# Kernel optimization log

Measured on AMD Instinct MI355X. Metric: run time of the kernel, lower is better.

## Reference

```python
import jax, jax.numpy as jnp
import numpy as np
from jax import lax

DIM = 96
B, S = 2, 48
EPS_LN = 1e-6
EPS_GRN = 1e-6


def setup_inputs() -> dict:
    key = jax.random.key(0)
    ks = jax.random.split(key, 11)
    d, h = DIM, 4 * DIM
    return {
        "x": jax.random.normal(ks[0], (B, d, S, S, S), jnp.float32),
        "dw_w": jax.random.normal(ks[1], (d, 1, 7, 7, 7), jnp.float32) * 0.05,  # (O, I/groups, kD,kH,kW)
        "dw_b": jax.random.normal(ks[2], (d,), jnp.float32) * 0.02,
        "ln_w": jnp.ones((d,), jnp.float32),
        "ln_b": jnp.zeros((d,), jnp.float32),
        "w1": jax.random.normal(ks[3], (d, h), jnp.float32) * 0.02,
        "b1": jax.random.normal(ks[4], (h,), jnp.float32) * 0.02,
        "grn_w": jax.random.normal(ks[5], (h,), jnp.float32) * 0.02,
        "grn_b": jax.random.normal(ks[6], (h,), jnp.float32) * 0.02,
        "w2": jax.random.normal(ks[7], (h, d), jnp.float32) * 0.02,
        "b2": jax.random.normal(ks[8], (d,), jnp.float32) * 0.02,
    }


def reference(x, dw_w, dw_b, ln_w, ln_b, w1, b1, grn_w, grn_b, w2, b2):
    # depthwise 7x7x7 conv, padding 3, groups = channels; x: (B, C, D, H, W)
    y = lax.conv_general_dilated(
        x, dw_w, window_strides=(1, 1, 1), padding=[(3, 3)] * 3,
        dimension_numbers=("NCDHW", "OIDHW", "NCDHW"), feature_group_count=DIM,
    ) + dw_b[None, :, None, None, None]
    # channels_last: (B, D, H, W, C)
    h = jnp.transpose(y, (0, 2, 3, 4, 1))
    # LayerNorm over channel dim
    mu = jnp.mean(h, axis=-1, keepdims=True)
    var = jnp.mean((h - mu) ** 2, axis=-1, keepdims=True)
    h = (h - mu) * lax.rsqrt(var + EPS_LN) * ln_w + ln_b
    # pointwise MLP expand + GELU (exact, erf-based, like torch)
    h = jnp.einsum("bdhwc,ce->bdhwe", h, w1) + b1
    h = jax.nn.gelu(h, approximate=False)
    # GRN: global L2 norm over spatial dims (1,2,3), per channel
    g = jnp.sqrt(jnp.sum(h * h, axis=(1, 2, 3), keepdims=True))  # (B,1,1,1,4C)
    n = g / (jnp.mean(g, axis=-1, keepdims=True) + EPS_GRN)
    h = grn_w * (h * n) + grn_b + h
    # pointwise MLP contract
    h = jnp.einsum("bdhwe,ec->bdhwc", h, w2) + b2
    # back to channels_first + residual
    return x + jnp.transpose(h, (0, 4, 1, 2, 3))
```

## Files before the change

kernel.cpp:

```cpp
#include <hip/hip_runtime.h>
#include <hip/hip_bf16.h>
#include <string.h>

#define S3 110592
#define CDIM 96
#define EDIM 384
#define ZIN 14
#define YIN 22

typedef __attribute__((ext_vector_type(8))) short bf16x8;
typedef __attribute__((ext_vector_type(4))) float f32x4;
typedef unsigned short ushort_t;
typedef unsigned char uchar_t;

__device__ __forceinline__ ushort_t f2bf(float f) {
  __hip_bfloat16 h = __float2bfloat16(f);
  union { __hip_bfloat16 h; ushort_t u; } cv; cv.h = h; return cv.u;
}
__device__ __forceinline__ float bf2f(ushort_t u) {
  union { __hip_bfloat16 h; ushort_t u; } cv; cv.u = u; return __bfloat162float(cv.h);
}
__device__ __forceinline__ uchar_t f2fp8(float f) {
  int r = __builtin_amdgcn_cvt_pk_fp8_f32(f, f, 0, false);
  return (uchar_t)(r & 0xff);
}
__device__ __forceinline__ float gelu_fast(float v) {
  float t = v * v;
  float u = v * fmaf(-0.10294324f, t, -2.3022084f);
  float s = __builtin_amdgcn_exp2f(u);
  return v * __builtin_amdgcn_rcpf(1.f + s);
}

__global__ void kprep(const float* __restrict__ ln_w, const float* __restrict__ ln_b,
                      const float* __restrict__ w1, const float* __restrict__ b1,
                      const float* __restrict__ grn_b, const float* __restrict__ w2,
                      const float* __restrict__ b2,
                      ushort_t* __restrict__ w1p, float* __restrict__ b1f, float* __restrict__ bias2) {
  int idx = blockIdx.x * 256 + threadIdx.x;
  if (idx < 24 * 3 * 64 * 8) {
    int j = idx & 7, lane = (idx >> 3) & 63, ks = (idx >> 9) % 3, nt = idx / 1536;
    int c = ks * 32 + (lane >> 4) * 8 + j;
    int e = nt * 16 + (lane & 15);
    w1p[idx] = f2bf(ln_w[c] * w1[c * EDIM + e]);
  }
  if (idx < EDIM) {
    float s = b1[idx];
    for (int c = 0; c < CDIM; ++c) s += ln_b[c] * w1[c * EDIM + idx];
    b1f[idx] = s;
  }
  if (idx < CDIM) {
    float s = b2[idx];
    for (int e = 0; e < EDIM; ++e) s += grn_b[e] * w2[e * CDIM + idx];
    bias2[idx] = s;
  }
}

__global__ void kpackB(const float* __restrict__ dw_w, ushort_t* __restrict__ Btab) {
  int base_i = (blockIdx.x * 256 + threadIdx.x) * 8;
  if (base_i >= 96 * 49 * 512) return;
  int pos = base_i & 511; int t = (base_i >> 9) % 49; int c = base_i / (49 * 512);
  int lane = pos >> 3;
  int k0 = (lane >> 4) * 8, n = lane & 15;
  int tz = t / 7, ty = t % 7;
  const float* w = dw_w + c * 343 + tz * 49 + ty * 7;
  ushort_t tmp[8];
#pragma unroll
  for (int j = 0; j < 8; ++j) {
    int tx = k0 + j - n - 1;
    tmp[j] = (tx >= 0 && tx < 7) ? f2bf(w[tx]) : (ushort_t)0;
  }
  *(uint4*)&Btab[base_i] = *(uint4*)tmp;
}

template<int HALF>
__device__ __forceinline__ void conv_ty_loop(const unsigned* tile, const ushort_t* Bt,
                                             int lane, int am, int xg, f32x4* acc) {
#pragma unroll 1
  for (int ty = 0; ty < 7; ++ty) {
    bf16x8 bfr[7];
#pragma unroll
    for (int tz = 0; tz < 7; ++tz)
      bfr[tz] = *(const bf16x8*)&Bt[(tz * 7 + ty) * 512 + lane * 8];
    int rowbase = am + ty;
#pragma unroll
    for (int zl = 0; zl < 7; ++zl) {
      int row = (HALF * 7 + zl) * YIN + rowbase;
      int byteoff = (row << 7) + (xg ^ ((row & 7) << 4));
      bf16x8 af = *(const bf16x8*)((const char*)tile + byteoff);
#pragma unroll
      for (int tz = 0; tz < 7; ++tz) {
        int l = (HALF == 0) ? (zl - tz) : (zl + 6 - tz);
        if (l >= 0 && l < 7)
          acc[l] = __builtin_amdgcn_mfma_f32_16x16x32_bf16(af, bfr[tz], acc[l], 0, 0, 0);
      }
    }
  }
}

__global__ __launch_bounds__(384, 6) void kconv(const float* __restrict__ x,
                                                const ushort_t* __restrict__ Btab,
                                                const float* __restrict__ dw_b,
                                                ushort_t* __restrict__ y) {
  __shared__ unsigned tile[ZIN * YIN * 32];
  int bid = blockIdx.x;
  int xcd = bid & 7, wi = bid >> 3;
  int c = xcd * 12 + wi / 36;
  int rr_ = wi % 36;
  int b = rr_ / 18;
  int t_ = rr_ % 18;
  int zt = t_ / 3, yt = t_ % 3;
  int z0 = zt * 8, y0 = yt * 16;
  size_t base = (size_t)(b * 96 + c) * S3;
  int tid = threadIdx.x;

  for (int i = tid; i < 308 * 8; i += 384) {
    int row = i >> 3; int pe = i & 7;
    int pc = (pe < 2) ? pe : pe + 24;
    tile[(row << 5) + (pc ^ ((row & 7) << 2))] = 0u;
  }
  {
    const float* xb = x + base;
#pragma unroll
    for (int hb = 0; hb < 2; ++hb) {
      float2 pv[10];
#pragma unroll
      for (int k = 0; k < 10; ++k) {
        int i = tid + (hb * 10 + k) * 384;
        i = (i < 7392) ? i : 7391;
        int row = i / 24; int pc = 2 + (i - row * 24);
        int dz = row / YIN, dy = row - dz * YIN;
        int gz = z0 - 3 + dz, gy = y0 - 3 + dy;
        int cz = min(max(gz, 0), 47), cy = min(max(gy, 0), 47);
        pv[k] = *(const float2*)&xb[(size_t)cz * 2304 + cy * 48 + 2 * pc - 4];
      }
#pragma unroll
      for (int k = 0; k < 10; ++k) {
        int i = tid + (hb * 10 + k) * 384;
        i = (i < 7392) ? i : 7391;
        int row = i / 24; int pc = 2 + (i - row * 24);
        int dz = row / YIN, dy = row - dz * YIN;
        int gz = z0 - 3 + dz, gy = y0 - 3 + dy;
        bool ok = ((unsigned)gz < 48u) && ((unsigned)gy < 48u);
        float v0 = ok ? pv[k].x : 0.f;
        float v1 = ok ? pv[k].y : 0.f;
        tile[(row << 5) + (pc ^ ((row & 7) << 2))] = (unsigned)f2bf(v0) | ((unsigned)f2bf(v1) << 16);
      }
    }
  }
  __syncthreads();

  int w = tid >> 6;
  int X = w % 3, half = w / 3;
  int lane = tid & 63;
  int am = lane & 15, g = lane >> 4;
  int xg = X * 32 + g * 16;

  f32x4 acc[7];
#pragma unroll
  for (int p = 0; p < 7; ++p) acc[p] = (f32x4){0.f, 0.f, 0.f, 0.f};

  const ushort_t* __restrict__ Bt = Btab + (size_t)c * 49 * 512;
  if (half == 0) conv_ty_loop<0>(tile, Bt, lane, am, xg, acc);
  else           conv_ty_loop<1>(tile, Bt, lane, am, xg, acc);

  float bv = dw_b[c];
  float* red = (float*)tile;
  int rcol = X * 16 + am;
  __syncthreads();
  if (half == 0) {
#pragma unroll
    for (int l = 1; l < 7; ++l)
#pragma unroll
      for (int r = 0; r < 4; ++r)
        red[(l - 1) * 800 + (g * 4 + r) * 50 + rcol] = acc[l][r];
  }
  __syncthreads();
  if (half == 0) {
    size_t zb = base + (size_t)z0 * 2304;
#pragma unroll
    for (int r = 0; r < 4; ++r)
      y[zb + (size_t)(y0 + g * 4 + r) * 48 + rcol] = f2bf(acc[0][r] + bv);
  } else {
#pragma unroll
    for (int l = 0; l < 7; ++l) {
      size_t zb = base + (size_t)(z0 + l + 1) * 2304;
#pragma unroll
      for (int r = 0; r < 4; ++r) {
        float v = acc[l][r] + bv;
        if (l < 6) v += red[l * 800 + (g * 4 + r) * 50 + rcol];
        y[zb + (size_t)(y0 + g * 4 + r) * 48 + rcol] = f2bf(v);
      }
    }
  }
}

__global__ __launch_bounds__(512, 4) void ksum(const ushort_t* __restrict__ y,
                                               const ushort_t* __restrict__ w1p,
                                               const float* __restrict__ b1f,
                                               float* __restrict__ sumsq,
                                               ushort_t* __restrict__ anorm) {
  __shared__ ushort_t Al[64 * 104];
  __shared__ float red_s[8][64], red_q[8][64];
  __shared__ float stat_mu[64], stat_rv[64];
  __shared__ float ssq_s[EDIM];
  int tid = threadIdx.x;
  int q = tid >> 6, lane = tid & 63;
  size_t pos0 = (size_t)blockIdx.x * 64;
  int b = (int)(pos0 / S3);
  int sp0 = (int)(pos0 % S3);

  bf16x8 bfg[3][3];
#pragma unroll
  for (int ntl = 0; ntl < 3; ++ntl)
#pragma unroll
    for (int ks = 0; ks < 3; ++ks)
      bfg[ntl][ks] = *(const bf16x8*)&w1p[(size_t)(((q * 3 + ntl) * 3 + ks) * 64 + lane) * 8];

  float v[12];
  float s = 0.f, ss = 0.f;
  const ushort_t* yb = y + (size_t)b * 96 * S3 + sp0 + lane;
#pragma unroll
  for (int i = 0; i < 12; ++i) {
    float f = bf2f(yb[(size_t)(q * 12 + i) * S3]);
    v[i] = f; s += f; ss += f * f;
  }
  red_s[q][lane] = s; red_q[q][lane] = ss;
  __syncthreads();
  if (tid < 64) {
    float su = 0.f, sq = 0.f;
#pragma unroll
    for (int k = 0; k < 8; ++k) { su += red_s[k][tid]; sq += red_q[k][tid]; }
    float mu = su * (1.f / 96.f);
    float var = sq * (1.f / 96.f) - mu * mu;
    stat_mu[tid] = mu;
    stat_rv[tid] = rsqrtf(var + 1e-6f);
  }
  __syncthreads();
  {
    float mu = stat_mu[lane], rv = stat_rv[lane];
#pragma unroll
    for (int i4 = 0; i4 < 3; ++i4) {
      ushort_t u0 = f2bf((v[i4 * 4 + 0] - mu) * rv);
      ushort_t u1 = f2bf((v[i4 * 4 + 1] - mu) * rv);
      ushort_t u2 = f2bf((v[i4 * 4 + 2] - mu) * rv);
      ushort_t u3 = f2bf((v[i4 * 4 + 3] - mu) * rv);
      uint2 t; t.x = (unsigned)u0 | ((unsigned)u1 << 16); t.y = (unsigned)u2 | ((unsigned)u3 << 16);
      *(uint2*)&Al[lane * 104 + q * 12 + i4 * 4] = t;
    }
  }
  __syncthreads();

  {
    uint4* dst = (uint4*)(anorm + pos0 * 96);
    for (int i = tid; i < 64 * 12; i += 512) {
      int p = i / 12, j = i - p * 12;
      dst[p * 12 + j] = *(const uint4*)&Al[p * 104 + j * 8];
    }
  }

  f32x4 acc[4][3];
#pragma unroll
  for (int mt = 0; mt < 4; ++mt)
#pragma unroll
    for (int ntl = 0; ntl < 3; ++ntl) acc[mt][ntl] = (f32x4){0.f, 0.f, 0.f, 0.f};

  int row = lane & 15, g = lane >> 4;
#pragma unroll
  for (int ks = 0; ks < 3; ++ks) {
    bf16x8 af[4];
    int colb = ks * 32 + g * 8;
#pragma unroll
    for (int mt = 0; mt < 4; ++mt)
      af[mt] = *(const bf16x8*)&Al[(mt * 16 + row) * 104 + colb];
#pragma unroll
    for (int ntl = 0; ntl < 3; ++ntl) {
#pragma unroll
      for (int mt = 0; mt < 4; ++mt)
        acc[mt][ntl] = __builtin_amdgcn_mfma_f32_16x16x32_bf16(af[mt], bfg[ntl][ks], acc[mt][ntl], 0, 0, 0);
    }
  }

#pragma unroll
  for (int ntl = 0; ntl < 3; ++ntl) {
    int e = q * 48 + ntl * 16 + row;
    float bb = b1f[e];
    float ssq = 0.f;
#pragma unroll
    for (int mt = 0; mt < 4; ++mt) {
#pragma unroll
      for (int r = 0; r < 4; ++r) {
        float gel = gelu_fast(acc[mt][ntl][r] + bb);
        ssq += gel * gel;
      }
    }
    ssq += __shfl_xor(ssq, 16, 64);
    ssq += __shfl_xor(ssq, 32, 64);
    if (g == 0) ssq_s[e] = ssq;
  }
  __syncthreads();
  if (tid < EDIM) atomicAdd(&sumsq[b * EDIM + tid], ssq_s[tid]);
}

__global__ void kscale(const float* __restrict__ sumsq, const float* __restrict__ grn_w,
                       float* __restrict__ scale) {
  __shared__ float wsum[6];
  __shared__ float mean_s;
  int b = blockIdx.x, e = threadIdx.x;
  float gv = sqrtf(sumsq[b * EDIM + e]);
  float t = gv;
#pragma unroll
  for (int off = 1; off <= 32; off <<= 1) t += __shfl_xor(t, off, 64);
  if ((e & 63) == 0) wsum[e >> 6] = t;
  __syncthreads();
  if (e == 0) {
    float m = 0.f;
    for (int i = 0; i < 6; ++i) m += wsum[i];
    mean_s = m * (1.f / EDIM);
  }
  __syncthreads();
  scale[b * EDIM + e] = grn_w[e] * (gv / (mean_s + 1e-6f)) + 1.f;
}

__global__ void kpackw2(const float* __restrict__ scale, const float* __restrict__ w2,
                        uchar_t* __restrict__ w2s) {
  int idx = blockIdx.x * 256 + threadIdx.x;
  if (idx >= 9216) return;
  int lane = idx & 63;
  int ks = (idx >> 6) % 12;
  int nt = ((idx >> 6) / 12) % 6;
  int b = idx / 4608;
  int cc = nt * 16 + (lane & 15);
  float sw[8];
#pragma unroll
  for (int j = 0; j < 8; ++j) {
    int e = ks * 32 + (lane >> 4) * 8 + j;
    sw[j] = scale[b * EDIM + e] * w2[e * CDIM + cc];
  }
  unsigned r0 = (unsigned)__builtin_amdgcn_cvt_pk_fp8_f32(sw[0], sw[1], 0, false);
  r0 = (unsigned)__builtin_amdgcn_cvt_pk_fp8_f32(sw[2], sw[3], (int)r0, true);
  unsigned r1 = (unsigned)__builtin_amdgcn_cvt_pk_fp8_f32(sw[4], sw[5], 0, false);
  r1 = (unsigned)__builtin_amdgcn_cvt_pk_fp8_f32(sw[6], sw[7], (int)r1, true);
  *(uint2*)&w2s[(size_t)((b * 72 + nt * 12 + ks) * 64 + lane) * 8] = make_uint2(r0, r1);
}

__global__ __launch_bounds__(512, 6) void kfused(const ushort_t* __restrict__ anorm,
                                                 const ushort_t* __restrict__ w1p,
                                                 const float* __restrict__ b1f,
                                                 const uchar_t* __restrict__ w2s,
                                                 const float* __restrict__ bias2,
                                                 const float* __restrict__ x,
                                                 float* __restrict__ out) {
  __shared__ __align__(16) uchar_t htile[64 * 400];

  int tid = threadIdx.x;
  int q = tid >> 6, lane = tid & 63;
  size_t pos0 = (size_t)blockIdx.x * 64;
  int b = (int)(pos0 / S3);
  int sp0 = (int)(pos0 % S3);
  int row = lane & 15, g = lane >> 4;
  int mt2 = q & 3, nh = q >> 2;

  f32x4 xv[3];
  float bb2[3];
#pragma unroll
  for (int ntl = 0; ntl < 3; ++ntl) {
    int cc = (nh * 3 + ntl) * 16 + row;
    xv[ntl] = *(const f32x4*)&x[(size_t)(b * 96 + cc) * S3 + sp0 + mt2 * 16 + g * 4];
    bb2[ntl] = bias2[cc];
  }

  f32x4 acc[4][3];
#pragma unroll
  for (int mt = 0; mt < 4; ++mt)
#pragma unroll
    for (int ntl = 0; ntl < 3; ++ntl) acc[mt][ntl] = (f32x4){0.f, 0.f, 0.f, 0.f};

  const ushort_t* ab = anorm + pos0 * 96;
#pragma unroll
  for (int ks = 0; ks < 3; ++ks) {
    int colb = ks * 32 + g * 8;
    bf16x8 af[4];
#pragma unroll
    for (int mt = 0; mt < 4; ++mt)
      af[mt] = *(const bf16x8*)&ab[(mt * 16 + row) * 96 + colb];
#pragma unroll
    for (int ntl = 0; ntl < 3; ++ntl) {
      bf16x8 bfg = *(const bf16x8*)&w1p[(size_t)(((q * 3 + ntl) * 3 + ks) * 64 + lane) * 8];
#pragma unroll
      for (int mt = 0; mt < 4; ++mt)
        acc[mt][ntl] = __builtin_amdgcn_mfma_f32_16x16x32_bf16(af[mt], bfg, acc[mt][ntl], 0, 0, 0);
    }
  }

#pragma unroll
  for (int ntl = 0; ntl < 3; ++ntl) {
    int e = q * 48 + ntl * 16 + row;
    float bb = b1f[e];
#pragma unroll
    for (int mt = 0; mt < 4; ++mt) {
#pragma unroll
      for (int r = 0; r < 4; ++r) {
        float gel = gelu_fast(acc[mt][ntl][r] + bb);
        htile[(mt * 16 + g * 4 + r) * 400 + e] = f2fp8(gel);
      }
    }
  }
  __syncthreads();

  f32x4 acc2[3];
#pragma unroll
  for (int ntl = 0; ntl < 3; ++ntl) acc2[ntl] = (f32x4){0.f, 0.f, 0.f, 0.f};
  const uchar_t* w2b = w2s + (size_t)b * 36864;
  const uchar_t* arow = &htile[(mt2 * 16 + row) * 400];
#pragma unroll
  for (int ks = 0; ks < 12; ++ks) {
    long af8 = *(const long*)&arow[g * 8 + ks * 32];
#pragma unroll
    for (int ntl = 0; ntl < 3; ++ntl) {
      int nt = nh * 3 + ntl;
      long bf8 = *(const long*)&w2b[(size_t)((nt * 12 + ks) * 64 + lane) * 8];
      acc2[ntl] = __builtin_amdgcn_mfma_f32_16x16x32_fp8_fp8(af8, bf8, acc2[ntl], 0, 0, 0);
    }
  }

#pragma unroll
  for (int ntl = 0; ntl < 3; ++ntl) {
    int cc = (nh * 3 + ntl) * 16 + row;
    f32x4 ov;
#pragma unroll
    for (int r = 0; r < 4; ++r) ov[r] = acc2[ntl][r] + bb2[ntl] + xv[ntl][r];
    *(f32x4*)&out[(size_t)(b * 96 + cc) * S3 + sp0 + mt2 * 16 + g * 4] = ov;
  }
}

extern "C" void kernel_launch(void* const* d_in, const int* in_sizes, int n_in,
                              void* d_out, int out_size, void* d_ws, size_t ws_size,
                              hipStream_t stream) {
  const float* x     = (const float*)d_in[0];
  const float* dw_w  = (const float*)d_in[1];
  const float* dw_b  = (const float*)d_in[2];
  const float* ln_w  = (const float*)d_in[3];
  const float* ln_b  = (const float*)d_in[4];
  const float* w1    = (const float*)d_in[5];
  const float* b1    = (const float*)d_in[6];
  const float* grn_w = (const float*)d_in[7];
  const float* grn_b = (const float*)d_in[8];
  const float* w2    = (const float*)d_in[9];
  const float* b2    = (const float*)d_in[10];
  float* out = (float*)d_out;

  char* ws = (char*)d_ws;
  size_t off = 0;
  auto alloc = [&](size_t bytes) -> void* {
    void* p = ws + off;
    off = (off + bytes + 511) & ~(size_t)511;
    return p;
  };
  ushort_t* y     = (ushort_t*)alloc((size_t)2 * 96 * S3 * 2);
  ushort_t* anorm = (ushort_t*)alloc((size_t)221184 * 96 * 2);
  ushort_t* w1p   = (ushort_t*)alloc(36864 * 2);
  uchar_t* w2s    = (uchar_t*)alloc((size_t)2 * 36864);
  ushort_t* Btab  = (ushort_t*)alloc((size_t)96 * 49 * 512 * 2);
  float* b1f      = (float*)alloc(EDIM * 4);
  float* bias2    = (float*)alloc(CDIM * 4);
  float* sumsq    = (float*)alloc(2 * EDIM * 4);
  float* scale    = (float*)alloc(2 * EDIM * 4);

  hipMemsetAsync(sumsq, 0, 2 * EDIM * 4, stream);
  kprep<<<145, 256, 0, stream>>>(ln_w, ln_b, w1, b1, grn_b, w2, b2, w1p, b1f, bias2);
  kpackB<<<1176, 256, 0, stream>>>(dw_w, Btab);
  kconv<<<3456, 384, 0, stream>>>(x, Btab, dw_b, y);
  ksum<<<3456, 512, 0, stream>>>(y, w1p, b1f, sumsq, anorm);
  kscale<<<2, 384, 0, stream>>>(sumsq, grn_w, scale);
  kpackw2<<<36, 256, 0, stream>>>(scale, w2, w2s);
  kfused<<<3456, 512, 0, stream>>>(anorm, w1p, b1f, w2s, bias2, x, out);
}
```

Baseline: 286.8 us.

## Pre-convert input to bf16 and load conv halo tiles directly into LDS

```diff
diff --git a/kernel.cpp b/kernel.cpp
--- a/kernel.cpp
+++ b/kernel.cpp
@@ -8,6 +8,9 @@
 #define ZIN 14
 #define YIN 22
 
+#define AS1 __attribute__((address_space(1)))
+#define AS3 __attribute__((address_space(3)))
+
 typedef __attribute__((ext_vector_type(8))) short bf16x8;
 typedef __attribute__((ext_vector_type(4))) float f32x4;
 typedef unsigned short ushort_t;
@@ -29,6 +32,18 @@
   float u = v * fmaf(-0.10294324f, t, -2.3022084f);
   float s = __builtin_amdgcn_exp2f(u);
   return v * __builtin_amdgcn_rcpf(1.f + s);
+}
+
+__global__ __launch_bounds__(256) void kcvt(const float* __restrict__ x, ushort_t* __restrict__ xbf) {
+  size_t i = ((size_t)blockIdx.x * 256 + threadIdx.x) * 8;
+  f32x4 a = *(const f32x4*)&x[i];
+  f32x4 b = *(const f32x4*)&x[i + 4];
+  ushort_t t[8];
+#pragma unroll
+  for (int j = 0; j < 4; ++j) t[j] = f2bf(a[j]);
+#pragma unroll
+  for (int j = 0; j < 4; ++j) t[4 + j] = f2bf(b[j]);
+  *(uint4*)&xbf[i] = *(uint4*)t;
 }
 
 __global__ void kprep(const float* __restrict__ ln_w, const float* __restrict__ ln_b,
@@ -97,10 +112,11 @@
   }
 }
 
-__global__ __launch_bounds__(384, 6) void kconv(const float* __restrict__ x,
+__global__ __launch_bounds__(384, 6) void kconv(const ushort_t* __restrict__ xbf,
                                                 const ushort_t* __restrict__ Btab,
                                                 const float* __restrict__ dw_b,
-                                                ushort_t* __restrict__ y) {
+                                                ushort_t* __restrict__ y,
+                                                const unsigned* __restrict__ zerobuf) {
   __shared__ unsigned tile[ZIN * YIN * 32];
   int bid = blockIdx.x;
   int xcd = bid & 7, wi = bid >> 3;
@@ -113,38 +129,21 @@
   size_t base = (size_t)(b * 96 + c) * S3;
   int tid = threadIdx.x;
 
-  for (int i = tid; i < 308 * 8; i += 384) {
-    int row = i >> 3; int pe = i & 7;
-    int pc = (pe < 2) ? pe : pe + 24;
-    tile[(row << 5) + (pc ^ ((row & 7) << 2))] = 0u;
-  }
   {
-    const float* xb = x + base;
-#pragma unroll
-    for (int hb = 0; hb < 2; ++hb) {
-      float2 pv[10];
-#pragma unroll
-      for (int k = 0; k < 10; ++k) {
-        int i = tid + (hb * 10 + k) * 384;
-        i = (i < 7392) ? i : 7391;
-        int row = i / 24; int pc = 2 + (i - row * 24);
-        int dz = row / YIN, dy = row - dz * YIN;
-        int gz = z0 - 3 + dz, gy = y0 - 3 + dy;
-        int cz = min(max(gz, 0), 47), cy = min(max(gy, 0), 47);
-        pv[k] = *(const float2*)&xb[(size_t)cz * 2304 + cy * 48 + 2 * pc - 4];
-      }
-#pragma unroll
-      for (int k = 0; k < 10; ++k) {
-        int i = tid + (hb * 10 + k) * 384;
-        i = (i < 7392) ? i : 7391;
-        int row = i / 24; int pc = 2 + (i - row * 24);
-        int dz = row / YIN, dy = row - dz * YIN;
-        int gz = z0 - 3 + dz, gy = y0 - 3 + dy;
-        bool ok = ((unsigned)gz < 48u) && ((unsigned)gy < 48u);
-        float v0 = ok ? pv[k].x : 0.f;
-        float v1 = ok ? pv[k].y : 0.f;
-        tile[(row << 5) + (pc ^ ((row & 7) << 2))] = (unsigned)f2bf(v0) | ((unsigned)f2bf(v1) << 16);
-      }
+    const unsigned* xp = (const unsigned*)xbf + (size_t)(b * 96 + c) * 55296;
+    int wv = tid >> 6, lane_ = tid & 63;
+    int h = lane_ >> 5, wd = lane_ & 31;
+#pragma unroll 2
+    for (int ch = wv; ch < 154; ch += 6) {
+      int row = 2 * ch + h;
+      int dz = (row * 2979) >> 16;
+      int dy = row - 22 * dz;
+      int gz = z0 - 3 + dz, gy = y0 - 3 + dy;
+      int pc = wd ^ ((row & 7) << 2);
+      bool valid = ((unsigned)gz < 48u) & ((unsigned)gy < 48u) & ((unsigned)(pc - 2) < 24u);
+      const unsigned* src = valid ? (xp + (gz * 1152 + gy * 24 + (pc - 2))) : zerobuf;
+      __builtin_amdgcn_global_load_lds((const AS1 void*)src,
+                                       (AS3 void*)&tile[ch * 64], 4, 0, 0);
     }
   }
   __syncthreads();
@@ -348,7 +347,7 @@
                                                  const float* __restrict__ b1f,
                                                  const uchar_t* __restrict__ w2s,
                                                  const float* __restrict__ bias2,
-                                                 const float* __restrict__ x,
+                                                 const ushort_t* __restrict__ xbf,
                                                  float* __restrict__ out) {
   __shared__ __align__(16) uchar_t htile[64 * 400];
 
@@ -360,12 +359,12 @@
   int row = lane & 15, g = lane >> 4;
   int mt2 = q & 3, nh = q >> 2;
 
-  f32x4 xv[3];
+  uint2 xr[3];
   float bb2[3];
 #pragma unroll
   for (int ntl = 0; ntl < 3; ++ntl) {
     int cc = (nh * 3 + ntl) * 16 + row;
-    xv[ntl] = *(const f32x4*)&x[(size_t)(b * 96 + cc) * S3 + sp0 + mt2 * 16 + g * 4];
+    xr[ntl] = *(const uint2*)&xbf[(size_t)(b * 96 + cc) * S3 + sp0 + mt2 * 16 + g * 4];
     bb2[ntl] = bias2[cc];
   }
 
@@ -426,9 +425,14 @@
 #pragma unroll
   for (int ntl = 0; ntl < 3; ++ntl) {
     int cc = (nh * 3 + ntl) * 16 + row;
+    float xf[4];
+    xf[0] = bf2f((ushort_t)(xr[ntl].x & 0xffff));
+    xf[1] = bf2f((ushort_t)(xr[ntl].x >> 16));
+    xf[2] = bf2f((ushort_t)(xr[ntl].y & 0xffff));
+    xf[3] = bf2f((ushort_t)(xr[ntl].y >> 16));
     f32x4 ov;
 #pragma unroll
-    for (int r = 0; r < 4; ++r) ov[r] = acc2[ntl][r] + bb2[ntl] + xv[ntl][r];
+    for (int r = 0; r < 4; ++r) ov[r] = acc2[ntl][r] + bb2[ntl] + xf[r];
     *(f32x4*)&out[(size_t)(b * 96 + cc) * S3 + sp0 + mt2 * 16 + g * 4] = ov;
   }
 }
@@ -458,6 +462,7 @@
   };
   ushort_t* y     = (ushort_t*)alloc((size_t)2 * 96 * S3 * 2);
   ushort_t* anorm = (ushort_t*)alloc((size_t)221184 * 96 * 2);
+  ushort_t* xbf   = (ushort_t*)alloc((size_t)2 * 96 * S3 * 2);
   ushort_t* w1p   = (ushort_t*)alloc(36864 * 2);
   uchar_t* w2s    = (uchar_t*)alloc((size_t)2 * 36864);
   ushort_t* Btab  = (ushort_t*)alloc((size_t)96 * 49 * 512 * 2);
@@ -465,13 +470,16 @@
   float* bias2    = (float*)alloc(CDIM * 4);
   float* sumsq    = (float*)alloc(2 * EDIM * 4);
   float* scale    = (float*)alloc(2 * EDIM * 4);
+  unsigned* zerobuf = (unsigned*)alloc(256);
 
   hipMemsetAsync(sumsq, 0, 2 * EDIM * 4, stream);
+  hipMemsetAsync(zerobuf, 0, 256, stream);
+  kcvt<<<10368, 256, 0, stream>>>(x, xbf);
   kprep<<<145, 256, 0, stream>>>(ln_w, ln_b, w1, b1, grn_b, w2, b2, w1p, b1f, bias2);
   kpackB<<<1176, 256, 0, stream>>>(dw_w, Btab);
-  kconv<<<3456, 384, 0, stream>>>(x, Btab, dw_b, y);
+  kconv<<<3456, 384, 0, stream>>>(xbf, Btab, dw_b, y, zerobuf);
   ksum<<<3456, 512, 0, stream>>>(y, w1p, b1f, sumsq, anorm);
   kscale<<<2, 384, 0, stream>>>(sumsq, grn_w, scale);
   kpackw2<<<36, 256, 0, stream>>>(scale, w2, w2s);
-  kfused<<<3456, 512, 0, stream>>>(anorm, w1p, b1f, w2s, bias2, x, out);
-}
+  kfused<<<3456, 512, 0, stream>>>(anorm, w1p, b1f, w2s, bias2, xbf, out);
+}
```

After: 316.0 us. 1.1x slower.
